# Kernel tuning notes

Measured on AMD Instinct MI355X. Metric: run time of the kernel, lower is better.

The kernel has to match this reference:

```python
import jax, jax.numpy as jnp
import numpy as np

K = 1e-3          # sigmoid temperature from MAPLoss(k=0.001): sigmoid(x) = 1/(1+exp(-x/K))
N, D = 512, 128   # batch of embeddings
NUM_CLASSES = 32
EPS = 1e-8


def setup_inputs() -> dict:
    key = jax.random.key(0)
    k1, k2 = jax.random.split(key)
    return {
        "input": jax.random.normal(k1, (N, D), dtype=jnp.float32),
        "target": jax.random.randint(k2, (N,), 0, NUM_CLASSES, dtype=jnp.int64),
    }


def _offdiag_cols(n):
    # cols[i, j] = j-th column index != i, in increasing order (matches
    # torch sm[~eye].view(n, n-1) row-major off-diagonal extraction)
    idx = jnp.arange(n - 1)[None, :]
    rows = jnp.arange(n)[:, None]
    return idx + (idx >= rows)  # [n, n-1] int


def reference(input, target):
    n = input.shape[0]
    # cosine similarity matrix
    norms = jnp.maximum(jnp.linalg.norm(input, axis=1, keepdims=True), EPS)
    xn = input / norms
    sm = xn @ xn.T  # [n, n]

    cols = _offdiag_cols(n)  # [n, n-1]
    ranking = jnp.take_along_axis(sm, cols, axis=1)  # [n, n-1]
    gt_full = (target[None, :] == target[:, None])    # [n, n] bool
    gt = jnp.take_along_axis(gt_full, cols, axis=1).astype(input.dtype)  # [n, n-1]

    # indicator[i, j, l] = sigmoid((r[i, l] - r[i, j]) / K)   -- O(n^3) cube
    indicator = jax.nn.sigmoid((ranking[:, None, :] - ranking[:, :, None]) / K)

    accumulated_gt = jnp.einsum('il,ijl->ij', gt, indicator)  # [n, n-1]
    denom = indicator.sum(-1) + 0.5                           # [n, n-1]
    prec = accumulated_gt / denom
    ap = jnp.sum(gt * prec, axis=1)    # [n]
    num_positives = gt.sum(-1)         # [n]

    valid = num_positives > 0
    ap_norm = jnp.where(valid, ap / jnp.where(valid, num_positives, 1.0), 0.0)
    n_valid = valid.sum().astype(input.dtype)
    return 1.0 - ap_norm.sum() / n_valid
```

## Files before the change

kernel.cpp:

```cpp
#include <hip/hip_runtime.h>

#define N 512
#define D 128
#define RS_SCALE 1442.6950408889634f
#define W_INV (1.0f / 18.0f)
#define B_OFF 1530.0f
#define PADV -1600.0f
#define NB 172

static __device__ __forceinline__ float rcp_fast(float x) {
    return __builtin_amdgcn_rcpf(x);
}
static __device__ __forceinline__ float exp2_fast(float x) {
    return __builtin_amdgcn_exp2f(x);
}

__global__ __launch_bounds__(256) void map_sim_kernel(
    const float* __restrict__ x, float* __restrict__ rs,
    int* __restrict__ ticket)
{
    const int bi = blockIdx.x;
    const int bj = blockIdx.y;
    const int t = threadIdx.x;
    __shared__ float As[16 * D];
    __shared__ float Bs[32 * D];

    if (bi == 0 && bj == 0 && t == 0) *ticket = 0;

#pragma unroll
    for (int s = 0; s < 2; ++s) {
        int ch = t + 256 * s;
        int row = ch >> 5, c4 = ch & 31;
        *(float4*)(As + row * D + ((c4 ^ row) << 2)) =
            *(const float4*)(x + (bi * 16 + row) * D + c4 * 4);
    }
#pragma unroll
    for (int s = 0; s < 4; ++s) {
        int ch = t + 256 * s;
        int row = ch >> 5, c4 = ch & 31;
        *(float4*)(Bs + row * D + ((c4 ^ row) << 2)) =
            *(const float4*)(x + (bj * 32 + row) * D + c4 * 4);
    }
    __syncthreads();

    const int c = t & 31;
    const int rp = t >> 5;
    const int ra0 = 2 * rp, ra1 = 2 * rp + 1;
    float acc0 = 0.f, acc1 = 0.f;
#pragma unroll 8
    for (int k4 = 0; k4 < D / 4; ++k4) {
        float4 b = *(const float4*)(Bs + c * D + ((k4 ^ c) << 2));
        float4 a0 = *(const float4*)(As + ra0 * D + ((k4 ^ ra0) << 2));
        float4 a1 = *(const float4*)(As + ra1 * D + ((k4 ^ ra1) << 2));
        acc0 = fmaf(a0.x, b.x, acc0); acc0 = fmaf(a0.y, b.y, acc0);
        acc0 = fmaf(a0.z, b.z, acc0); acc0 = fmaf(a0.w, b.w, acc0);
        acc1 = fmaf(a1.x, b.x, acc1); acc1 = fmaf(a1.y, b.y, acc1);
        acc1 = fmaf(a1.z, b.z, acc1); acc1 = fmaf(a1.w, b.w, acc1);
    }
    const int gc = bj * 32 + c;
    rs[(bi * 16 + ra0) * N + gc] = acc0;
    rs[(bi * 16 + ra1) * N + gc] = acc1;
}

__global__ __launch_bounds__(512) void map_ap_kernel(
    const float* __restrict__ rs, const int* __restrict__ tgt,
    float2* __restrict__ av, int* __restrict__ ticket,
    float* __restrict__ out)
{
    const int i = blockIdx.x, t = threadIdx.x;
    const int lane = t & 63;
    __shared__ int hist[256];
    __shared__ int offs[NB];
    __shared__ int wtot[4];
    __shared__ unsigned gbits[16];
    __shared__ __align__(16) float skey[N];
    __shared__ float red[16];
    __shared__ int amLast;

    const int ti = tgt[i];
    const float draw = rs[i * N + t];
    const float ssT = rs[t * N + t];
    const float ssI = rs[i * N + i];
    const int tgT = tgt[t];

    if (t < 256) hist[t] = 0;
    if (t < NB) offs[t] = 0;
    if (t < 16) gbits[t] = 0u;

    const bool self = (t == i);
    const float invT = rcp_fast(fmaxf(sqrtf(ssT), 1e-8f));
    const float invI = rcp_fast(fmaxf(sqrtf(ssI), 1e-8f));
    const float val = self ? PADV : draw * invT * invI * RS_SCALE;
    const int gti = (!self && tgT == ti) ? 1 : 0;
    int q = (int)((val + B_OFF) * W_INV);
    q = max(0, min(NB - 1, q));
    __syncthreads();
    atomicAdd(&hist[q], (1 << 10) | gti);
    __syncthreads();

    int v = (t < 256) ? hist[t] : 0;
#pragma unroll
    for (int off = 1; off < 64; off <<= 1) {
        int u = __shfl_up(v, off);
        if (lane >= off) v += u;
    }
    if (t < 256 && lane == 63) wtot[t >> 6] = v;
    __syncthreads();
    if (t < 256) {
        int w = t >> 6, add = 0;
        if (w > 0) add += wtot[0];
        if (w > 1) add += wtot[1];
        if (w > 2) add += wtot[2];
        hist[t] = v + add;
    }
    __syncthreads();

    {
        int base = (q > 0) ? (hist[q - 1] >> 10) : 0;
        int pos = base + atomicAdd(&offs[q], 1);
        skey[pos] = val;
        if (gti) atomicOr(&gbits[pos >> 5], 1u << (pos & 31));
    }
    __syncthreads();

    const int totGt = hist[NB - 1] & 1023;
    const float4* sk4 = (const float4*)skey;

    const float rj = skey[t];
    const float gtj = (float)((gbits[t >> 5] >> (t & 31)) & 1u);
    int qj = (int)((rj + B_OFF) * W_INV);
    qj = max(0, min(NB - 1, qj));
    const int gl = lane & 48;
    const int qlo = __shfl(qj, gl);
    const int qhi = __shfl(qj, gl + 15);
    const int lo = (qlo > 1) ? (hist[qlo - 2] >> 10) : 0;
    const int e1 = min(qhi + 1, NB - 1);
    const int hi = hist[e1] >> 10;

    float dsum = (float)(N - hi);
    float gsum = (float)(totGt - (hist[e1] & 1023));

    float d0 = 0.f, d1 = 0.f, d2 = 0.f, d3 = 0.f;
    float g0 = 0.f, g1 = 0.f, g2 = 0.f, g3 = 0.f;
    int k = lo & ~7;
    for (; k + 8 <= hi; k += 8) {
        float4 ka = sk4[k >> 2];
        float4 kb = sk4[(k >> 2) + 1];
        unsigned gw = (gbits[k >> 5] >> (k & 31)) & 0xffu;
        float s0 = rcp_fast(1.f + exp2_fast(rj - ka.x));
        float s1 = rcp_fast(1.f + exp2_fast(rj - ka.y));
        float s2 = rcp_fast(1.f + exp2_fast(rj - ka.z));
        float s3 = rcp_fast(1.f + exp2_fast(rj - ka.w));
        float s4 = rcp_fast(1.f + exp2_fast(rj - kb.x));
        float s5 = rcp_fast(1.f + exp2_fast(rj - kb.y));
        float s6 = rcp_fast(1.f + exp2_fast(rj - kb.z));
        float s7 = rcp_fast(1.f + exp2_fast(rj - kb.w));
        d0 += s0 + s4; d1 += s1 + s5; d2 += s2 + s6; d3 += s3 + s7;
        g0 += ((gw      ) & 1u) ? s0 : 0.f;
        g1 += ((gw >> 1u) & 1u) ? s1 : 0.f;
        g2 += ((gw >> 2u) & 1u) ? s2 : 0.f;
        g3 += ((gw >> 3u) & 1u) ? s3 : 0.f;
        g0 += ((gw >> 4u) & 1u) ? s4 : 0.f;
        g1 += ((gw >> 5u) & 1u) ? s5 : 0.f;
        g2 += ((gw >> 6u) & 1u) ? s6 : 0.f;
        g3 += ((gw >> 7u) & 1u) ? s7 : 0.f;
    }
    dsum += (d0 + d1) + (d2 + d3);
    gsum += (g0 + g1) + (g2 + g3);
    for (; k < hi; ++k) {
        float s = rcp_fast(1.f + exp2_fast(rj - skey[k]));
        dsum += s;
        gsum += ((gbits[k >> 5] >> (k & 31)) & 1u) ? s : 0.f;
    }

    float apAcc = gtj * gsum * rcp_fast(dsum + 0.5f);
    float npAcc = gtj;

#pragma unroll
    for (int off = 32; off; off >>= 1) {
        apAcc += __shfl_down(apAcc, off);
        npAcc += __shfl_down(npAcc, off);
    }
    if (lane == 0) { red[(t >> 6) * 2] = apAcc; red[(t >> 6) * 2 + 1] = npAcc; }
    __syncthreads();
    if (t == 0) {
        float A = 0.f, P = 0.f;
#pragma unroll
        for (int kk = 0; kk < 8; ++kk) { A += red[2 * kk]; P += red[2 * kk + 1]; }
        av[i] = make_float2((P > 0.f) ? (A * rcp_fast(P)) : 0.f,
                            (P > 0.f) ? 1.f : 0.f);
        __threadfence();
        int old = atomicAdd(ticket, 1);
        amLast = (old == (int)gridDim.x - 1) ? 1 : 0;
    }
    __syncthreads();

    if (amLast) {
        __threadfence();
        float2 p = av[t];
        float a = p.x, vv = p.y;
#pragma unroll
        for (int off = 32; off; off >>= 1) {
            a += __shfl_down(a, off);
            vv += __shfl_down(vv, off);
        }
        if (lane == 0) { red[(t >> 6) * 2] = a; red[(t >> 6) * 2 + 1] = vv; }
        __syncthreads();
        if (t == 0) {
            float A = 0.f, V = 0.f;
#pragma unroll
            for (int kk = 0; kk < 8; ++kk) { A += red[2 * kk]; V += red[2 * kk + 1]; }
            out[0] = 1.0f - A * rcp_fast(V);
        }
    }
}

extern "C" void kernel_launch(void* const* d_in, const int* in_sizes, int n_in,
                              void* d_out, int out_size, void* d_ws, size_t ws_size,
                              hipStream_t stream) {
    const float* x = (const float*)d_in[0];
    const int* tgt = (const int*)d_in[1];
    float* out = (float*)d_out;

    float* rs = (float*)d_ws;
    float2* av = (float2*)((char*)d_ws + N * N * 4);
    int* ticket = (int*)((char*)d_ws + N * N * 4 + N * 8);

    map_sim_kernel<<<dim3(32, 16), 256, 0, stream>>>(x, rs, ticket);
    map_ap_kernel<<<N, 512, 0, stream>>>(rs, tgt, av, ticket, out);
}
```

Measured before the change: 29.34 us.

## Compact positive keys into separate list and narrow histogram bins

Narrows the histogram bin width and raises the bin count so each wavefront's window of nearby keys needing an exact sigmoid shrinks. The positive-label gsum is taken out of the windowed loop and computed instead over a compacted array of ground-truth keys built with popcount prefix sums. This removes the per-element bitmask select from the hot loop. In exchange every thread now evaluates a sigmoid against all positives (about 16 on average), adds a compaction pass with an extra barrier, and assumes at most 64 positives per row via MAXGT.

```diff
diff --git a/kernel.cpp b/kernel.cpp
--- a/kernel.cpp
+++ b/kernel.cpp
@@ -3,10 +3,11 @@
 #define N 512
 #define D 128
 #define RS_SCALE 1442.6950408889634f
-#define W_INV (1.0f / 18.0f)
-#define B_OFF 1530.0f
+#define W_INV (1.0f / 11.0f)
+#define B_OFF 1444.0f
 #define PADV -1600.0f
-#define NB 172
+#define NB 256
+#define MAXGT 64
 
 static __device__ __forceinline__ float rcp_fast(float x) {
     return __builtin_amdgcn_rcpf(x);
@@ -69,11 +70,12 @@
 {
     const int i = blockIdx.x, t = threadIdx.x;
     const int lane = t & 63;
-    __shared__ int hist[256];
+    __shared__ int hist[NB];
     __shared__ int offs[NB];
     __shared__ int wtot[4];
     __shared__ unsigned gbits[16];
     __shared__ __align__(16) float skey[N];
+    __shared__ float gkey[MAXGT];
     __shared__ float red[16];
     __shared__ int amLast;
 
@@ -83,8 +85,7 @@
     const float ssI = rs[i * N + i];
     const int tgT = tgt[t];
 
-    if (t < 256) hist[t] = 0;
-    if (t < NB) offs[t] = 0;
+    if (t < NB) { hist[t] = 0; offs[t] = 0; }
     if (t < 16) gbits[t] = 0u;
 
     const bool self = (t == i);
@@ -98,15 +99,15 @@
     atomicAdd(&hist[q], (1 << 10) | gti);
     __syncthreads();
 
-    int v = (t < 256) ? hist[t] : 0;
+    int v = (t < NB) ? hist[t] : 0;
 #pragma unroll
     for (int off = 1; off < 64; off <<= 1) {
         int u = __shfl_up(v, off);
         if (lane >= off) v += u;
     }
-    if (t < 256 && lane == 63) wtot[t >> 6] = v;
-    __syncthreads();
-    if (t < 256) {
+    if (t < NB && lane == 63) wtot[t >> 6] = v;
+    __syncthreads();
+    if (t < NB) {
         int w = t >> 6, add = 0;
         if (w > 0) add += wtot[0];
         if (w > 1) add += wtot[1];
@@ -123,11 +124,22 @@
     }
     __syncthreads();
 
+    const unsigned myw = gbits[t >> 5];
+    const int mybit = (myw >> (t & 31)) & 1;
+    if (mybit) {
+        int r = __popc(myw & ((1u << (t & 31)) - 1u));
+#pragma unroll
+        for (int u = 0; u < 16; ++u)
+            if (u < (t >> 5)) r += __popc(gbits[u]);
+        gkey[r] = skey[t];
+    }
+    __syncthreads();
+
     const int totGt = hist[NB - 1] & 1023;
     const float4* sk4 = (const float4*)skey;
 
     const float rj = skey[t];
-    const float gtj = (float)((gbits[t >> 5] >> (t & 31)) & 1u);
+    const float gtj = (float)mybit;
     int qj = (int)((rj + B_OFF) * W_INV);
     qj = max(0, min(NB - 1, qj));
     const int gl = lane & 48;
@@ -138,40 +150,28 @@
     const int hi = hist[e1] >> 10;
 
     float dsum = (float)(N - hi);
-    float gsum = (float)(totGt - (hist[e1] & 1023));
 
     float d0 = 0.f, d1 = 0.f, d2 = 0.f, d3 = 0.f;
-    float g0 = 0.f, g1 = 0.f, g2 = 0.f, g3 = 0.f;
     int k = lo & ~7;
     for (; k + 8 <= hi; k += 8) {
         float4 ka = sk4[k >> 2];
         float4 kb = sk4[(k >> 2) + 1];
-        unsigned gw = (gbits[k >> 5] >> (k & 31)) & 0xffu;
-        float s0 = rcp_fast(1.f + exp2_fast(rj - ka.x));
-        float s1 = rcp_fast(1.f + exp2_fast(rj - ka.y));
-        float s2 = rcp_fast(1.f + exp2_fast(rj - ka.z));
-        float s3 = rcp_fast(1.f + exp2_fast(rj - ka.w));
-        float s4 = rcp_fast(1.f + exp2_fast(rj - kb.x));
-        float s5 = rcp_fast(1.f + exp2_fast(rj - kb.y));
-        float s6 = rcp_fast(1.f + exp2_fast(rj - kb.z));
-        float s7 = rcp_fast(1.f + exp2_fast(rj - kb.w));
-        d0 += s0 + s4; d1 += s1 + s5; d2 += s2 + s6; d3 += s3 + s7;
-        g0 += ((gw      ) & 1u) ? s0 : 0.f;
-        g1 += ((gw >> 1u) & 1u) ? s1 : 0.f;
-        g2 += ((gw >> 2u) & 1u) ? s2 : 0.f;
-        g3 += ((gw >> 3u) & 1u) ? s3 : 0.f;
-        g0 += ((gw >> 4u) & 1u) ? s4 : 0.f;
-        g1 += ((gw >> 5u) & 1u) ? s5 : 0.f;
-        g2 += ((gw >> 6u) & 1u) ? s6 : 0.f;
-        g3 += ((gw >> 7u) & 1u) ? s7 : 0.f;
+        d0 += rcp_fast(1.f + exp2_fast(rj - ka.x));
+        d1 += rcp_fast(1.f + exp2_fast(rj - ka.y));
+        d2 += rcp_fast(1.f + exp2_fast(rj - ka.z));
+        d3 += rcp_fast(1.f + exp2_fast(rj - ka.w));
+        d0 += rcp_fast(1.f + exp2_fast(rj - kb.x));
+        d1 += rcp_fast(1.f + exp2_fast(rj - kb.y));
+        d2 += rcp_fast(1.f + exp2_fast(rj - kb.z));
+        d3 += rcp_fast(1.f + exp2_fast(rj - kb.w));
     }
     dsum += (d0 + d1) + (d2 + d3);
-    gsum += (g0 + g1) + (g2 + g3);
-    for (; k < hi; ++k) {
-        float s = rcp_fast(1.f + exp2_fast(rj - skey[k]));
-        dsum += s;
-        gsum += ((gbits[k >> 5] >> (k & 31)) & 1u) ? s : 0.f;
-    }
+    for (; k < hi; ++k)
+        dsum += rcp_fast(1.f + exp2_fast(rj - skey[k]));
+
+    float gsum = 0.f;
+    for (int r = 0; r < totGt; ++r)
+        gsum += rcp_fast(1.f + exp2_fast(rj - gkey[r]));
 
     float apAcc = gtj * gsum * rcp_fast(dsum + 0.5f);
     float npAcc = gtj;
```

After: 27.99 us. -4.6%, faster.
